# Kernel optimization log

Measured on AMD Instinct MI355X. Metric: run time of the kernel, lower is better.

## Reference

```python
import jax, jax.numpy as jnp
import numpy as np

T = 17            # tensor side -> 289 flat channels
C = T * T
EPS = 1e-5


def tconv(x, W1, W2, b, stride):
    """Tucker-2 tensor conv: per offset (i,j) OUT = W1[i,j] @ X @ W2[i,j].
    x: [B, a*bt, H, W]; W1: [kh,kw,T,a]; W2: [kh,kw,bt,T]; b: [289].
    Equivalent dense kernel K[(p,q),(a,b),i,j] = W1[i,j,p,a]*W2[i,j,b,q]."""
    kh, kw, _, a = W1.shape
    bt = W2.shape[2]
    K = jnp.einsum('ijpa,ijbq->pqabij', W1, W2).reshape(C, a * bt, kh, kw)
    pad = (kh - 1) // 2
    y = jax.lax.conv_general_dilated(
        x, K, (stride, stride), [(pad, pad), (pad, pad)],
        dimension_numbers=('NCHW', 'OIHW', 'NCHW'))
    return y + b.reshape(1, C, 1, 1)


def bn(x, g, bta):
    # training-mode BN over flattened 17x17 tensor channels (biased var)
    m = jnp.mean(x, axis=(0, 2, 3), keepdims=True)
    v = jnp.var(x, axis=(0, 2, 3), keepdims=True)
    return g.reshape(1, -1, 1, 1) * (x - m) * jax.lax.rsqrt(v + EPS) + bta.reshape(1, -1, 1, 1)


def prelu(x, a):
    return jnp.where(x >= 0, x, a * x)


def setup_inputs() -> dict:
    key = jax.random.key(0)
    ks = jax.random.split(key, 8)
    x = jax.random.normal(ks[0], (32, 3, 160, 160), dtype=jnp.float32)
    s = 0.1
    feat_W1 = jax.random.normal(ks[1], (3, 3, T, 3), dtype=jnp.float32) * s
    feat_W2 = jax.random.normal(ks[2], (3, 3, 1, T), dtype=jnp.float32) * s
    feat_b = jnp.zeros((C,), dtype=jnp.float32)
    # 27 1x1 convs: shortcuts 0..8, block k uses 9+2k and 10+2k
    c11_W1 = jax.random.normal(ks[3], (27, 1, 1, T, T), dtype=jnp.float32) * s
    c11_W2 = jax.random.normal(ks[4], (27, 1, 1, T, T), dtype=jnp.float32) * s
    c11_b = jnp.zeros((27, C), dtype=jnp.float32)
    # 9 3x3 convs (one per block)
    c33_W1 = jax.random.normal(ks[5], (9, 3, 3, T, T), dtype=jnp.float32) * s
    c33_W2 = jax.random.normal(ks[6], (9, 3, 3, T, T), dtype=jnp.float32) * s
    c33_b = jnp.zeros((9, C), dtype=jnp.float32)
    # 37 BNs: 0=features, 1+j shortcut j, 10+3k..12+3k block k
    bn_g = jnp.ones((37, C), dtype=jnp.float32)
    bn_bt = jnp.zeros((37, C), dtype=jnp.float32)
    # 19 PReLUs: 0=features, block k uses 1+2k, 2+2k
    prelu_a = jnp.full((19,), 0.25, dtype=jnp.float32)
    return {"x": x, "feat_W1": feat_W1, "feat_W2": feat_W2, "feat_b": feat_b,
            "c11_W1": c11_W1, "c11_W2": c11_W2, "c11_b": c11_b,
            "c33_W1": c33_W1, "c33_W2": c33_W2, "c33_b": c33_b,
            "bn_g": bn_g, "bn_bt": bn_bt, "prelu_a": prelu_a}


def reference(x, feat_W1, feat_W2, feat_b, c11_W1, c11_W2, c11_b,
              c33_W1, c33_W2, c33_b, bn_g, bn_bt, prelu_a):
    # features: 3x3 s2 tensor conv [3,1]->[17,17], BN, PReLU
    h = tconv(x, feat_W1, feat_W2, feat_b, 2)
    h = prelu(bn(h, bn_g[0], bn_bt[0]), prelu_a[0])
    # 9 residual blocks; blocks 0,1 downsample by 2
    for k in range(9):
        s = 2 if k < 2 else 1
        i1, i2 = 9 + 2 * k, 10 + 2 * k
        j = 10 + 3 * k
        idn = bn(tconv(h, c11_W1[k], c11_W2[k], c11_b[k], s), bn_g[1 + k], bn_bt[1 + k])
        y = prelu(bn(tconv(h, c11_W1[i1], c11_W2[i1], c11_b[i1], 1), bn_g[j], bn_bt[j]), prelu_a[1 + 2 * k])
        y = prelu(bn(tconv(y, c33_W1[k], c33_W2[k], c33_b[k], s), bn_g[j + 1], bn_bt[j + 1]), prelu_a[2 + 2 * k])
        y = bn(tconv(y, c11_W1[i2], c11_W2[i2], c11_b[i2], 1), bn_g[j + 2], bn_bt[j + 2])
        h = y + idn
    return h  # [B, 289, 20, 20] == torch [B,1,20,20,17,17] flattened
```

## Files before the change

### kernel.cpp

```cpp
#include <hip/hip_runtime.h>
#include <hip/hip_bf16.h>

#define EPS 1e-5f
#define NB 256
#define CSTR 292
#define PST 580

typedef __hip_bfloat16 bf16;
typedef short s16x8 __attribute__((ext_vector_type(8)));
typedef float f32x4 __attribute__((ext_vector_type(4)));
typedef unsigned short u16x4 __attribute__((ext_vector_type(4)));
typedef unsigned short u16x8 __attribute__((ext_vector_type(8)));

__device__ inline float bf2f(unsigned short u) {
    union { unsigned int i; float f; } z; z.i = ((unsigned int)u) << 16; return z.f;
}
__device__ inline unsigned short f2bf(float f) {
    union { bf16 h; unsigned short u; } z; z.h = __float2bfloat16(f); return z.u;
}
__device__ inline unsigned short f2bf_trunc(float f) {
    union { float f; unsigned int u; } z; z.f = f; return (unsigned short)(z.u >> 16);
}
__device__ inline float ldv(const bf16* p, long i) { return __bfloat162float(p[i]); }
__device__ inline float ldv(const float* p, long i) { return p[i]; }

__device__ __forceinline__ void prep_frag(const float* w1, const float* w2,
                                          bf16* o, int kt, int nt, int l) {
#pragma unroll
    for (int e = 0; e < 8; ++e) {
        int k = kt * 32 + ((l >> 4) << 3) + e;
        int n = nt * 16 + (l & 15);
        float v = 0.f;
        if (k < 289 && n < 289)
            v = w1[(n / 17) * 17 + (k / 17)] * w2[(k % 17) * 17 + (n % 17)];
        o[e] = __float2bfloat16(v);
    }
}

__global__ void prep11_all_k(const float* __restrict__ W1all, const float* __restrict__ W2all,
                             bf16* __restrict__ Bsw) {
    int bi = blockIdx.x;
    int cv = bi / 190, r = bi - cv * 190;
    int kt = r / 19, nt = r - kt * 19;
    prep_frag(W1all + (size_t)cv * 289, W2all + (size_t)cv * 289,
              Bsw + (size_t)bi * 512 + threadIdx.x * 8, kt, nt, threadIdx.x);
}

__global__ void prep33_k(const float* __restrict__ W1, const float* __restrict__ W2,
                         bf16* __restrict__ Bsw) {
    int bi = blockIdx.x;
    int tap = bi / 190; int r = bi - tap * 190;
    int kt = r / 19, nt = r - kt * 19;
    prep_frag(W1 + (size_t)tap * 289, W2 + (size_t)tap * 289,
              Bsw + (size_t)bi * 512 + threadIdx.x * 8, kt, nt, threadIdx.x);
}

__global__ void prep33all_k(const float* __restrict__ W1, const float* __restrict__ W2,
                            bf16* __restrict__ Bsw) {
    int fi = blockIdx.x * 4 + (threadIdx.x >> 6);
    int l = threadIdx.x & 63;
    int kb = fi / 1710, r = fi - kb * 1710;
    int tap = r / 190; int rr = r - tap * 190;
    int kt = rr / 19, nt = rr - kt * 19;
    const float* w1 = W1 + (long)(kb + 1) * 9 * 289 + (long)tap * 289;
    const float* w2 = W2 + (long)(kb + 1) * 9 * 289 + (long)tap * 289;
    prep_frag(w1, w2, Bsw + (size_t)fi * 512 + l * 8, kt, nt, l);
}

__global__ void feat_k(const float* __restrict__ x, bf16* __restrict__ out,
                       const float* __restrict__ W1, const float* __restrict__ W2) {
    __shared__ float W1s[459], W2s[153];
    int tid = threadIdx.x;
    for (int i = tid; i < 459; i += 256) W1s[i] = W1[i];
    for (int i = tid; i < 153; i += 256) W2s[i] = W2[i];
    __syncthreads();
    const long N = 204800L * 17;
    for (long idx = (long)blockIdx.x * 256 + tid; idx < N; idx += 524288L) {
        int pix = (int)(idx / 17), p = (int)(idx - (long)pix * 17);
        int b = pix / 6400; int rr = pix - b * 6400;
        int oh = rr / 80, ow = rr - oh * 80;
        float y[17];
#pragma unroll
        for (int q = 0; q < 17; ++q) y[q] = 0.f;
        for (int di = 0; di < 3; ++di) {
            int ih = oh * 2 + di - 1;
            if (ih < 0 || ih >= 160) continue;
            for (int dj = 0; dj < 3; ++dj) {
                int iw = ow * 2 + dj - 1;
                if (iw < 0 || iw >= 160) continue;
                int k = di * 3 + dj;
                long xb = (long)b * 76800 + ih * 160 + iw;
                float dot = W1s[(k * 17 + p) * 3 + 0] * x[xb]
                          + W1s[(k * 17 + p) * 3 + 1] * x[xb + 25600]
                          + W1s[(k * 17 + p) * 3 + 2] * x[xb + 51200];
#pragma unroll
                for (int q = 0; q < 17; ++q) y[q] += dot * W2s[k * 17 + q];
            }
        }
        long op = (long)pix * CSTR + p * 17;
#pragma unroll
        for (int q = 0; q < 17; ++q) out[op + q] = __float2bfloat16(y[q]);
    }
}

template <typename TI, typename TO, int TAPS, bool DUAL, int MT>
__global__ __launch_bounds__(256, MT == 2 ? 3 : 5) void gemm_k(
    const TI* __restrict__ in1, const TI* __restrict__ in2, TO* __restrict__ out,
    const bf16* __restrict__ Bs, const float* __restrict__ scshAll, int bn1, int bn2,
    const float* __restrict__ alphaPtr, float* __restrict__ partial,
    int Hin, int Win, int Hout, int Wout, int stride) {
    constexpr int MROWS = 16 * MT;
    constexpr int SITS = (37 * MROWS + 255) / 256;
    static_assert(MROWS * 304 * sizeof(TO) <= 2 * MROWS * 640, "epilogue must fit As");
    __shared__ char As[2 * MROWS * 640];
    __shared__ float sc1[296], sh1[296];
    __shared__ float sc2[DUAL ? 296 : 1], sh2[DUAL ? 296 : 1];
    __shared__ long gb00[MROWS];
    __shared__ int ihw0[MROWS];
    int tid = threadIdx.x;
    int HWin = Hin * Win, HWout = Hout * Wout;
    int pix0 = blockIdx.x * MROWS;
    for (int i = tid; i < 296; i += 256) {
        int cc = i < 289 ? i : 0;
        sc1[i] = scshAll[bn1 * 578 + cc]; sh1[i] = scshAll[bn1 * 578 + 289 + cc];
        if constexpr (DUAL) {
            sc2[i] = scshAll[bn2 * 578 + cc]; sh2[i] = scshAll[bn2 * 578 + 289 + cc];
        }
    }
    if (tid < MROWS) {
        int op = pix0 + tid;
        int b = op / HWout; int rr = op - b * HWout;
        int oh = rr / Wout, ow = rr - oh * Wout;
        int ih0 = oh * stride + (TAPS == 9 ? -1 : 0);
        int iw0 = ow * stride + (TAPS == 9 ? -1 : 0);
        gb00[tid] = ((long)b * HWin + (long)ih0 * Win + iw0) * CSTR;
        ihw0[tid] = ((ih0 + 1) << 16) | (iw0 + 1);
    }
    if (tid < 8 * MROWS) {
        int half = tid / (4 * MROWS), r = (tid >> 2) & (MROWS - 1), c = tid & 3;
        int byte = (r * 640 + 576 + c * 16) ^ ((r & 7) << 4);
        *(u16x8*)(As + half * (MROWS * 640) + byte) = (u16x8){0, 0, 0, 0, 0, 0, 0, 0};
    }
    float alpha = DUAL ? 0.f : *alphaPtr;
    int w = tid >> 6, l = tid & 63;
    int nt0 = w * 5;
    int lane_n = l & 15;
    int kbyte = (l >> 4) << 4;
    f32x4 acc[MT][5];
#pragma unroll
    for (int m = 0; m < MT; ++m)
#pragma unroll
        for (int j = 0; j < 5; ++j) acc[m][j] = (f32x4){0.f, 0.f, 0.f, 0.f};
    __syncthreads();

    bool cact[SITS]; int cih[SITS], ciw[SITS], cwb[SITS], ck0[SITS]; long cgb[SITS];
#pragma unroll
    for (int it = 0; it < SITS; ++it) {
        int cid = it * 256 + tid;
        cact[it] = cid < 37 * MROWS;
        int row = cact[it] ? cid / 37 : 0;
        int j = cid - row * 37;
        ck0[it] = j * 8;
        cgb[it] = gb00[row] + j * 8;
        int pk = ihw0[row];
        cih[it] = (pk >> 16) - 1; ciw[it] = (pk & 0xffff) - 1;
        cwb[it] = (row * 640 + j * 16) ^ ((row & 7) << 4);
    }
    bool vld[SITS];
    u16x4 rh1[SITS][2]; f32x4 rf1[SITS][2];
    u16x4 rh2[DUAL ? SITS : 1][2]; f32x4 rf2[DUAL ? SITS : 1][2];

    auto LOAD = [&](int tap) {
        int di = (TAPS == 9) ? tap / 3 : 0;
        int dj = (TAPS == 9) ? tap - di * 3 : 0;
        long toff = (long)(di * Win + dj) * CSTR;
#pragma unroll
        for (int it = 0; it < SITS; ++it) {
            vld[it] = false;
            if (cact[it]) {
                int ih = cih[it] + di, iw = ciw[it] + dj;
                if (ih >= 0 && ih < Hin && iw >= 0 && iw < Win) {
                    vld[it] = true;
                    long gb = cgb[it] + toff;
                    if constexpr (sizeof(TI) == 2) {
                        rh1[it][0] = *(const u16x4*)((const bf16*)in1 + gb);
                        rh1[it][1] = *(const u16x4*)((const bf16*)in1 + gb + 4);
                        if constexpr (DUAL) {
                            rh2[it][0] = *(const u16x4*)((const bf16*)in2 + gb);
                            rh2[it][1] = *(const u16x4*)((const bf16*)in2 + gb + 4);
                        }
                    } else {
                        rf1[it][0] = *(const f32x4*)((const float*)in1 + gb);
                        rf1[it][1] = *(const f32x4*)((const float*)in1 + gb + 4);
                        if constexpr (DUAL) {
                            rf2[it][0] = *(const f32x4*)((const float*)in2 + gb);
                            rf2[it][1] = *(const f32x4*)((const float*)in2 + gb + 4);
                        }
                    }
                }
            }
        }
    };

    auto WRITE = [&]() {
#pragma unroll
        for (int it = 0; it < SITS; ++it) {
            if (!cact[it]) continue;
            float v[8];
            if (vld[it]) {
                int k0 = ck0[it];
                float r[8];
                if constexpr (sizeof(TI) == 2) {
#pragma unroll
                    for (int e = 0; e < 4; ++e) {
                        r[e] = bf2f(rh1[it][0][e]); r[4 + e] = bf2f(rh1[it][1][e]);
                    }
                } else {
#pragma unroll
                    for (int e = 0; e < 4; ++e) {
                        r[e] = rf1[it][0][e]; r[4 + e] = rf1[it][1][e];
                    }
                }
#pragma unroll
                for (int e = 0; e < 8; ++e) v[e] = sc1[k0 + e] * r[e] + sh1[k0 + e];
                if constexpr (DUAL) {
                    float q[8];
                    if constexpr (sizeof(TI) == 2) {
#pragma unroll
                        for (int e = 0; e < 4; ++e) {
                            q[e] = bf2f(rh2[it][0][e]); q[4 + e] = bf2f(rh2[it][1][e]);
                        }
                    } else {
#pragma unroll
                        for (int e = 0; e < 4; ++e) {
                            q[e] = rf2[it][0][e]; q[4 + e] = rf2[it][1][e];
                        }
                    }
#pragma unroll
                    for (int e = 0; e < 8; ++e) v[e] += sc2[k0 + e] * q[e] + sh2[k0 + e];
                } else {
#pragma unroll
                    for (int e = 0; e < 8; ++e) v[e] = v[e] >= 0.f ? v[e] : alpha * v[e];
                }
#pragma unroll
                for (int e = 0; e < 8; ++e) if (ck0[it] + e > 288) v[e] = 0.f;
            } else {
#pragma unroll
                for (int e = 0; e < 8; ++e) v[e] = 0.f;
            }
            u16x4 hi0, hi1, lo0, lo1;
#pragma unroll
            for (int e = 0; e < 4; ++e) {
                unsigned short h = f2bf(v[e]);
                hi0[e] = h; lo0[e] = f2bf_trunc(v[e] - bf2f(h));
                unsigned short h2 = f2bf(v[4 + e]);
                hi1[e] = h2; lo1[e] = f2bf_trunc(v[4 + e] - bf2f(h2));
            }
            int byte = cwb[it];
            *(u16x4*)(As + byte) = hi0;
            *(u16x4*)(As + byte + 8) = hi1;
            *(u16x4*)(As + MROWS * 640 + byte) = lo0;
            *(u16x4*)(As + MROWS * 640 + byte + 8) = lo1;
        }
    };

    LOAD(0);
#pragma unroll 1
    for (int tap = 0; tap < TAPS; ++tap) {
        WRITE();
        if (tap + 1 < TAPS) LOAD(tap + 1);
        __syncthreads();
        const bf16* bp = Bs + (size_t)tap * 97280 + (size_t)l * 8;
        int swz = (lane_n & 7) << 4;
        __builtin_amdgcn_s_setprio(1);
#pragma unroll 2
        for (int kt = 0; kt < 10; ++kt) {
            s16x8 ah[MT], al[MT];
#pragma unroll
            for (int m = 0; m < MT; ++m) {
                int ro = ((m * 16 + lane_n) * 640 + kbyte + kt * 64) ^ swz;
                ah[m] = *(const s16x8*)(As + ro);
                al[m] = *(const s16x8*)(As + MROWS * 640 + ro);
            }
#pragma unroll
            for (int j = 0; j < 5; ++j) {
                if (j < 4 || w < 3) {
                    s16x8 bfr = *(const s16x8*)(bp + (size_t)(kt * 19 + nt0 + j) * 512);
#pragma unroll
                    for (int m = 0; m < MT; ++m) {
                        acc[m][j] = __builtin_amdgcn_mfma_f32_16x16x32_bf16(
                            ah[m], bfr, acc[m][j], 0, 0, 0);
                        acc[m][j] = __builtin_amdgcn_mfma_f32_16x16x32_bf16(
                            al[m], bfr, acc[m][j], 0, 0, 0);
                    }
                }
            }
        }
        __builtin_amdgcn_s_setprio(0);
        __syncthreads();
    }
    {
#pragma unroll
        for (int j = 0; j < 5; ++j) {
            float s = 0.f, ss = 0.f;
            if (j < 4 || w < 3) {
#pragma unroll
                for (int m = 0; m < MT; ++m)
#pragma unroll
                    for (int e = 0; e < 4; ++e) {
                        float v = acc[m][j][e];
                        s += v; ss += v * v;
                    }
            }
            s += __shfl_xor(s, 16); ss += __shfl_xor(ss, 16);
            s += __shfl_xor(s, 32); ss += __shfl_xor(ss, 32);
            int n = (nt0 + j) * 16 + lane_n;
            if (l < 16 && n < 289 && (j < 4 || w < 3)) {
                partial[(long)blockIdx.x * PST + n] = s;
                partial[(long)blockIdx.x * PST + 290 + n] = ss;
            }
        }
    }
    {
        TO* ep = (TO*)As;
        int re = (l >> 4) << 2;
#pragma unroll
        for (int m = 0; m < MT; ++m) {
#pragma unroll
            for (int j = 0; j < 5; ++j) {
                if (j < 4 || w < 3) {
                    int n = (nt0 + j) * 16 + lane_n;
#pragma unroll
                    for (int e = 0; e < 4; ++e) {
                        if constexpr (sizeof(TO) == 2)
                            ep[(m * 16 + re + e) * 304 + n] = __float2bfloat16(acc[m][j][e]);
                        else
                            ((float*)ep)[(m * 16 + re + e) * 304 + n] = acc[m][j][e];
                    }
                }
            }
        }
        __syncthreads();
        for (int cid = tid; cid < MROWS * 73; cid += 256) {
            int row = cid / 73, j = cid - row * 73;
            long g = (long)(pix0 + row) * CSTR + j * 4;
            if constexpr (sizeof(TO) == 2) {
                u16x4 v = *(const u16x4*)((const bf16*)ep + row * 304 + j * 4);
                *(u16x4*)((bf16*)out + g) = v;
            } else {
                f32x4 v = *(const f32x4*)((const float*)ep + row * 304 + j * 4);
                *(f32x4*)((float*)out + g) = v;
            }
        }
    }
}

__global__ __launch_bounds__(256, 3) void gemm2_k(
    const float* __restrict__ in1, const float* __restrict__ in2,
    float* __restrict__ out1, float* __restrict__ out2,
    const bf16* __restrict__ Bs1, const bf16* __restrict__ Bs2,
    const float* __restrict__ scshAll, int bn1, int bn2,
    float* __restrict__ partial1, float* __restrict__ partial2) {
    constexpr int MROWS = 16;
    __shared__ char As[2 * MROWS * 640];
    __shared__ float sc1[296], sh1[296], sc2[296], sh2[296];
    int tid = threadIdx.x;
    for (int i = tid; i < 296; i += 256) {
        int cc = i < 289 ? i : 0;
        sc1[i] = scshAll[bn1 * 578 + cc]; sh1[i] = scshAll[bn1 * 578 + 289 + cc];
        sc2[i] = scshAll[bn2 * 578 + cc]; sh2[i] = scshAll[bn2 * 578 + 289 + cc];
    }
    if (tid < 128) {
        int half = tid >> 6, r = (tid >> 2) & 15, c = tid & 3;
        int byte = (r * 640 + 576 + c * 16) ^ ((r & 7) << 4);
        *(u16x8*)(As + half * (MROWS * 640) + byte) = (u16x8){0, 0, 0, 0, 0, 0, 0, 0};
    }
    int pix0 = blockIdx.x * MROWS;
    int w = tid >> 6, l = tid & 63;
    int nt0 = w * 5, lane_n = l & 15, kbyte = (l >> 4) << 4;
    f32x4 acc1[5], acc2[5];
#pragma unroll
    for (int j = 0; j < 5; ++j) {
        acc1[j] = (f32x4){0.f, 0.f, 0.f, 0.f};
        acc2[j] = (f32x4){0.f, 0.f, 0.f, 0.f};
    }
    __syncthreads();
#pragma unroll
    for (int it = 0; it < 3; ++it) {
        int cid = it * 256 + tid;
        if (cid < 592) {
            int row = cid / 37, j = cid - row * 37, k0 = j * 8;
            long gb = (long)(pix0 + row) * CSTR + k0;
            f32x4 a = *(const f32x4*)(in1 + gb), b = *(const f32x4*)(in1 + gb + 4);
            f32x4 c = *(const f32x4*)(in2 + gb), d = *(const f32x4*)(in2 + gb + 4);
            float v[8];
#pragma unroll
            for (int e = 0; e < 4; ++e) {
                v[e] = sc1[k0 + e] * a[e] + sh1[k0 + e] + sc2[k0 + e] * c[e] + sh2[k0 + e];
                v[4 + e] = sc1[k0 + 4 + e] * b[e] + sh1[k0 + 4 + e]
                         + sc2[k0 + 4 + e] * d[e] + sh2[k0 + 4 + e];
            }
#pragma unroll
            for (int e = 0; e < 8; ++e) if (k0 + e > 288) v[e] = 0.f;
            u16x4 hi0, hi1, lo0, lo1;
#pragma unroll
            for (int e = 0; e < 4; ++e) {
                unsigned short h = f2bf(v[e]);
                hi0[e] = h; lo0[e] = f2bf_trunc(v[e] - bf2f(h));
                unsigned short h2 = f2bf(v[4 + e]);
                hi1[e] = h2; lo1[e] = f2bf_trunc(v[4 + e] - bf2f(h2));
            }
            int byte = (row * 640 + j * 16) ^ ((row & 7) << 4);
            *(u16x4*)(As + byte) = hi0;
            *(u16x4*)(As + byte + 8) = hi1;
            *(u16x4*)(As + MROWS * 640 + byte) = lo0;
            *(u16x4*)(As + MROWS * 640 + byte + 8) = lo1;
        }
    }
    __syncthreads();
    const bf16* bp1 = Bs1 + (size_t)l * 8;
    const bf16* bp2 = Bs2 + (size_t)l * 8;
    int swz = (lane_n & 7) << 4;
    __builtin_amdgcn_s_setprio(1);
#pragma unroll 2
    for (int kt = 0; kt < 10; ++kt) {
        int ro = (lane_n * 640 + kbyte + kt * 64) ^ swz;
        s16x8 ah = *(const s16x8*)(As + ro);
        s16x8 al = *(const s16x8*)(As + MROWS * 640 + ro);
#pragma unroll
        for (int j = 0; j < 5; ++j) {
            if (j < 4 || w < 3) {
                size_t fo = (size_t)(kt * 19 + nt0 + j) * 512;
                s16x8 b1 = *(const s16x8*)(bp1 + fo);
                acc1[j] = __builtin_amdgcn_mfma_f32_16x16x32_bf16(ah, b1, acc1[j], 0, 0, 0);
                acc1[j] = __builtin_amdgcn_mfma_f32_16x16x32_bf16(al, b1, acc1[j], 0, 0, 0);
                s16x8 b2 = *(const s16x8*)(bp2 + fo);
                acc2[j] = __builtin_amdgcn_mfma_f32_16x16x32_bf16(ah, b2, acc2[j], 0, 0, 0);
                acc2[j] = __builtin_amdgcn_mfma_f32_16x16x32_bf16(al, b2, acc2[j], 0, 0, 0);
            }
        }
    }
    __builtin_amdgcn_s_setprio(0);
    __syncthreads();
#pragma unroll
    for (int j = 0; j < 5; ++j) {
        float s1 = 0.f, q1 = 0.f, s2 = 0.f, q2 = 0.f;
        if (j < 4 || w < 3) {
#pragma unroll
            for (int e = 0; e < 4; ++e) {
                float v1 = acc1[j][e]; s1 += v1; q1 += v1 * v1;
                float v2 = acc2[j][e]; s2 += v2; q2 += v2 * v2;
            }
        }
        s1 += __shfl_xor(s1, 16); q1 += __shfl_xor(q1, 16);
        s1 += __shfl_xor(s1, 32); q1 += __shfl_xor(q1, 32);
        s2 += __shfl_xor(s2, 16); q2 += __shfl_xor(q2, 16);
        s2 += __shfl_xor(s2, 32); q2 += __shfl_xor(q2, 32);
        int n = (nt0 + j) * 16 + lane_n;
        if (l < 16 && n < 289 && (j < 4 || w < 3)) {
            partial1[(long)blockIdx.x * PST + n] = s1;
            partial1[(long)blockIdx.x * PST + 290 + n] = q1;
            partial2[(long)blockIdx.x * PST + n] = s2;
            partial2[(long)blockIdx.x * PST + 290 + n] = q2;
        }
    }
    float* ep = (float*)As;
    int re = (l >> 4) << 2;
#pragma unroll
    for (int pass = 0; pass < 2; ++pass) {
        const f32x4* ac = pass ? acc2 : acc1;
        float* op = pass ? out2 : out1;
#pragma unroll
        for (int j = 0; j < 5; ++j) {
            if (j < 4 || w < 3) {
                int n = (nt0 + j) * 16 + lane_n;
#pragma unroll
                for (int e = 0; e < 4; ++e) ep[(re + e) * 304 + n] = ac[j][e];
            }
        }
        __syncthreads();
        for (int cid = tid; cid < MROWS * 73; cid += 256) {
            int row = cid / 73, j = cid - row * 73;
            long g = (long)(pix0 + row) * CSTR + j * 4;
            f32x4 v = *(const f32x4*)(ep + row * 304 + j * 4);
            *(f32x4*)(op + g) = v;
        }
        __syncthreads();
    }
}

__global__ void stats_k(const bf16* __restrict__ t, float* __restrict__ partial, int npix) {
    int c = threadIdx.x;
    if (c >= 289) return;
    float s = 0.f, ss = 0.f;
    for (int pix = blockIdx.x; pix < npix; pix += NB) {
        float v = ldv(t, (long)pix * CSTR + c);
        s += v; ss += v * v;
    }
    partial[(long)blockIdx.x * PST + c] = s;
    partial[(long)blockIdx.x * PST + 290 + c] = ss;
}

__device__ __forceinline__ void fin_one(const float* partial, const float* g,
                                        const float* bt, float* scshAll,
                                        int bnid, float invN, int GN, int c) {
    float s = 0.f, ss = 0.f;
    for (int k = threadIdx.x; k < GN; k += 256) {
        s += partial[(long)k * PST + c];
        ss += partial[(long)k * PST + 290 + c];
    }
    for (int o = 32; o; o >>= 1) { s += __shfl_down(s, o); ss += __shfl_down(ss, o); }
    __shared__ float ls[4], lss[4];
    int w = threadIdx.x >> 6;
    if ((threadIdx.x & 63) == 0) { ls[w] = s; lss[w] = ss; }
    __syncthreads();
    if (threadIdx.x == 0) {
        s = ls[0] + ls[1] + ls[2] + ls[3];
        ss = lss[0] + lss[1] + lss[2] + lss[3];
        float m = s * invN;
        float v = ss * invN - m * m;
        float sc = g[c] * rsqrtf(v + EPS);
        scshAll[bnid * 578 + c] = sc;
        scshAll[bnid * 578 + 289 + c] = bt[c] - m * sc;
    }
}

__global__ void finalize_k(const float* __restrict__ partial, const float* __restrict__ g,
                           const float* __restrict__ bt, float* __restrict__ scshAll,
                           int bnid, float invN, int GN) {
    fin_one(partial, g, bt, scshAll, bnid, invN, GN, blockIdx.x);
}

__global__ void finalize2v_k(const float* __restrict__ pA, const float* __restrict__ pB,
                             const float* __restrict__ gAll, const float* __restrict__ btAll,
                             float* __restrict__ scshAll, int bnA, int bnB,
                             float invA, int GNa, float invB, int GNb) {
    int q = blockIdx.x / 289, c = blockIdx.x - q * 289;
    const float* p = q ? pB : pA;
    int bnid = q ? bnB : bnA;
    fin_one(p, gAll + bnid * 289, btAll + bnid * 289, scshAll, bnid,
            q ? invB : invA, q ? GNb : GNa, c);
}

__global__ void final_k(const float* __restrict__ y3, const float* __restrict__ idn,
                        float* __restrict__ out, const float* __restrict__ scshAll,
                        int bnY, int bnI) {
    __shared__ float T[32][305];
    int bi = blockIdx.x;
    int b = bi / 13, t0 = (bi - (bi / 13) * 13) * 32;
    int tid = threadIdx.x;
    int nhw = 400 - t0; if (nhw > 32) nhw = 32;
    for (int idx = tid; idx < 32 * 304; idx += 256) {
        int hwl = idx / 304, c = idx - hwl * 304;
        float v = 0.f;
        if (hwl < nhw && c < 289) {
            long pix = (long)b * 400 + t0 + hwl;
            v = scshAll[bnY * 578 + c] * y3[pix * CSTR + c] + scshAll[bnY * 578 + 289 + c]
              + scshAll[bnI * 578 + c] * idn[pix * CSTR + c] + scshAll[bnI * 578 + 289 + c];
        }
        T[hwl][c] = v;
    }
    __syncthreads();
    for (int idx = tid; idx < 289 * 32; idx += 256) {
        int c = idx >> 5, hwl = idx & 31;
        if (hwl < nhw)
            out[((long)b * 289 + c) * 400 + t0 + hwl] = T[hwl][c];
    }
}

extern "C" void kernel_launch(void* const* d_in, const int* in_sizes, int n_in,
                              void* d_out, int out_size, void* d_ws, size_t ws_size,
                              hipStream_t stream) {
    const float* x     = (const float*)d_in[0];
    const float* fW1   = (const float*)d_in[1];
    const float* fW2   = (const float*)d_in[2];
    const float* c11W1 = (const float*)d_in[4];
    const float* c11W2 = (const float*)d_in[5];
    const float* c33W1 = (const float*)d_in[7];
    const float* c33W2 = (const float*)d_in[8];
    const float* bng   = (const float*)d_in[10];
    const float* bnbt  = (const float*)d_in[11];
    const float* pa    = (const float*)d_in[12];
    float* outp = (float*)d_out;

    char* base = (char*)d_ws;
    bf16*  A    = (bf16*)base;
    bf16*  Bb   = (bf16*)(base + 119603200L);
    bf16*  Cb   = (bf16*)(base + 149504000L);
    float* scsh = (float*)(base + 179404800L);
    bf16*  B33s = (bf16*)(base + 179490368L);
    size_t need = 181241408L;
    if (ws_size < need) return;
    float* D = (float*)base;
    float* E = (float*)(base + 14950400L);
    float* F = (float*)(base + 29900800L);
    float* partialA = (float*)(base + 50000000L);
    bf16*  B33all   = (bf16*)(base + 100000000L);

    float* partial = (float*)d_out;
    bf16*  B11all  = (bf16*)((char*)d_out + 7424000L);
    float* partial2 = partial + 800L * PST;
    float* partialBig = (float*)Cb;

    const float inv80 = 1.f / 204800.f, inv40 = 1.f / 51200.f, inv20 = 1.f / 12800.f;

#define B11(cv) (B11all + (size_t)(cv) * 97280)
#define B33A(cv) (B33all + (size_t)((cv) - 1) * 875520)
#define FIN(P, bnid, invN, GN) finalize_k<<<dim3(289), dim3(256), 0, stream>>>( \
        (P), bng + (bnid) * 289, bnbt + (bnid) * 289, scsh, (bnid), (invN), (GN))

    prep11_all_k<<<dim3(27 * 190), dim3(64), 0, stream>>>(c11W1, c11W2, B11all);

    feat_k<<<dim3(2048), dim3(256), 0, stream>>>(x, A, fW1, fW2);
    stats_k<<<dim3(NB), dim3(320), 0, stream>>>(A, partial, 204800);
    FIN(partial, 0, inv80, NB);

    gemm_k<bf16, bf16, 1, false, 2><<<dim3(1600), dim3(256), 0, stream>>>(
        A, nullptr, Bb, B11(0), scsh, 0, 0, pa + 0, partial, 80, 80, 40, 40, 2);
    gemm_k<bf16, bf16, 1, false, 2><<<dim3(6400), dim3(256), 0, stream>>>(
        A, nullptr, A, B11(9), scsh, 0, 0, pa + 0, partialBig, 80, 80, 80, 80, 1);
    finalize2v_k<<<dim3(578), dim3(256), 0, stream>>>(
        partial, partialBig, bng, bnbt, scsh, 1, 10, inv40, 1600, inv80, 6400);
    prep33_k<<<dim3(1710), dim3(64), 0, stream>>>(c33W1, c33W2, B33s);
    gemm_k<bf16, bf16, 9, false, 2><<<dim3(1600), dim3(256), 0, stream>>>(
        A, nullptr, Cb, B33s, scsh, 10, 0, pa + 1, partial, 80, 80, 40, 40, 2);
    prep33all_k<<<dim3(3420), dim3(256), 0, stream>>>(c33W1, c33W2, B33all);
    FIN(partial, 11, inv40, 1600);
    gemm_k<bf16, bf16, 1, false, 2><<<dim3(1600), dim3(256), 0, stream>>>(
        Cb, nullptr, Cb, B11(10), scsh, 11, 0, pa + 2, partial, 40, 40, 40, 40, 1);
    FIN(partial, 12, inv40, 1600);

    gemm_k<bf16, float, 1, true, 1><<<dim3(800), dim3(256), 0, stream>>>(
        Cb, Bb, D, B11(1), scsh, 12, 1, nullptr, partialA, 40, 40, 20, 20, 2);
    gemm_k<bf16, bf16, 1, true, 2><<<dim3(1600), dim3(256), 0, stream>>>(
        Cb, Bb, Cb, B11(11), scsh, 12, 1, nullptr, partial, 40, 40, 40, 40, 1);
    finalize2v_k<<<dim3(578), dim3(256), 0, stream>>>(
        partialA, partial, bng, bnbt, scsh, 2, 13, inv20, 800, inv40, 1600);
    gemm_k<bf16, float, 9, false, 2><<<dim3(400), dim3(256), 0, stream>>>(
        Cb, nullptr, E, B33A(1), scsh, 13, 0, pa + 3, partial, 40, 40, 20, 20, 2);
    FIN(partial, 14, inv20, 400);
    gemm_k<float, float, 1, false, 1><<<dim3(800), dim3(256), 0, stream>>>(
        E, nullptr, E, B11(12), scsh, 14, 0, pa + 4, partial, 20, 20, 20, 20, 1);
    FIN(partial, 15, inv20, 800);

    float *X = E, *Y = D, *Z = F;
    for (int k = 2; k < 9; ++k) {
        gemm2_k<<<dim3(800), dim3(256), 0, stream>>>(
            X, Y, Z, X, B11(k), B11(9 + 2 * k), scsh, 9 + 3 * k, k, partial, partial2);
        finalize2v_k<<<dim3(578), dim3(256), 0, stream>>>(
            partial, partial2, bng, bnbt, scsh, 1 + k, 10 + 3 * k,
            inv20, 800, inv20, 800);
        gemm_k<float, float, 9, false, 2><<<dim3(400), dim3(256), 0, stream>>>(
            X, nullptr, Y, B33A(k), scsh, 10 + 3 * k, 0, pa + 1 + 2 * k, partial,
            20, 20, 20, 20, 1);
        FIN(partial, 11 + 3 * k, inv20, 400);
        gemm_k<float, float, 1, false, 1><<<dim3(800), dim3(256), 0, stream>>>(
            Y, nullptr, Y, B11(10 + 2 * k), scsh, 11 + 3 * k, 0, pa + 2 + 2 * k, partial,
            20, 20, 20, 20, 1);
        FIN(partial, 12 + 3 * k, inv20, 800);
        float* t = X; X = Y; Y = Z; Z = t;
    }
    final_k<<<dim3(416), dim3(256), 0, stream>>>(X, Y, outp, scsh, 36, 9);
}
```

Measured before the change: 2.214 ms.

## Fuse first BN statistics into feature conv and stage output through LDS

The feature tensor conv now accumulates per-channel sum and sum-of-squares in registers while it computes, reduces them through shared-memory atomics, and writes per-block partials. The separate stats kernel, which re-read the whole 204800x292 bf16 activation, is removed. Outputs are staged in a shared tile of 15 pixels and written with coalesced 8-byte stores instead of scattered 2-byte stores. The trade-off is more partials (2048 instead of 256) for finalize to reduce, extra barriers per tile, and one of 256 threads left idle.

```diff
diff --git a/kernel.cpp b/kernel.cpp
--- a/kernel.cpp
+++ b/kernel.cpp
@@ -2,9 +2,9 @@
 #include <hip/hip_bf16.h>
 
 #define EPS 1e-5f
-#define NB 256
 #define CSTR 292
 #define PST 580
+#define FPIX 15
 
 typedef __hip_bfloat16 bf16;
 typedef short s16x8 __attribute__((ext_vector_type(8)));
@@ -21,8 +21,6 @@
 __device__ inline unsigned short f2bf_trunc(float f) {
     union { float f; unsigned int u; } z; z.f = f; return (unsigned short)(z.u >> 16);
 }
-__device__ inline float ldv(const bf16* p, long i) { return __bfloat162float(p[i]); }
-__device__ inline float ldv(const float* p, long i) { return p[i]; }
 
 __device__ __forceinline__ void prep_frag(const float* w1, const float* w2,
                                           bf16* o, int kt, int nt, int l) {
@@ -67,39 +65,77 @@
     prep_frag(w1, w2, Bsw + (size_t)fi * 512 + l * 8, kt, nt, l);
 }
 
-__global__ void feat_k(const float* __restrict__ x, bf16* __restrict__ out,
-                       const float* __restrict__ W1, const float* __restrict__ W2) {
+__global__ __launch_bounds__(256) void feat_k(
+    const float* __restrict__ x, bf16* __restrict__ out,
+    const float* __restrict__ W1, const float* __restrict__ W2,
+    float* __restrict__ partial) {
     __shared__ float W1s[459], W2s[153];
+    __shared__ float S[289], SS[289];
+    __shared__ bf16 T[FPIX][292];
     int tid = threadIdx.x;
     for (int i = tid; i < 459; i += 256) W1s[i] = W1[i];
     for (int i = tid; i < 153; i += 256) W2s[i] = W2[i];
-    __syncthreads();
-    const long N = 204800L * 17;
-    for (long idx = (long)blockIdx.x * 256 + tid; idx < N; idx += 524288L) {
-        int pix = (int)(idx / 17), p = (int)(idx - (long)pix * 17);
-        int b = pix / 6400; int rr = pix - b * 6400;
-        int oh = rr / 80, ow = rr - oh * 80;
-        float y[17];
-#pragma unroll
-        for (int q = 0; q < 17; ++q) y[q] = 0.f;
-        for (int di = 0; di < 3; ++di) {
-            int ih = oh * 2 + di - 1;
-            if (ih < 0 || ih >= 160) continue;
-            for (int dj = 0; dj < 3; ++dj) {
-                int iw = ow * 2 + dj - 1;
-                if (iw < 0 || iw >= 160) continue;
-                int k = di * 3 + dj;
-                long xb = (long)b * 76800 + ih * 160 + iw;
-                float dot = W1s[(k * 17 + p) * 3 + 0] * x[xb]
-                          + W1s[(k * 17 + p) * 3 + 1] * x[xb + 25600]
-                          + W1s[(k * 17 + p) * 3 + 2] * x[xb + 51200];
-#pragma unroll
-                for (int q = 0; q < 17; ++q) y[q] += dot * W2s[k * 17 + q];
-            }
-        }
-        long op = (long)pix * CSTR + p * 17;
-#pragma unroll
-        for (int q = 0; q < 17; ++q) out[op + q] = __float2bfloat16(y[q]);
+    for (int i = tid; i < 289; i += 256) { S[i] = 0.f; SS[i] = 0.f; }
+    if (tid < FPIX * 3) T[tid / 3][289 + tid % 3] = __float2bfloat16(0.f);
+    int lp = tid / 17, p = tid - lp * 17;
+    bool act = tid < 255;
+    float sacc[17], qacc[17];
+#pragma unroll
+    for (int q = 0; q < 17; ++q) { sacc[q] = 0.f; qacc[q] = 0.f; }
+    const int NT = (204800 + FPIX - 1) / FPIX;
+    __syncthreads();
+    for (int t = blockIdx.x; t < NT; t += gridDim.x) {
+        int pix0 = t * FPIX;
+        int pix = pix0 + lp;
+        if (act && pix < 204800) {
+            int b = pix / 6400; int rr = pix - b * 6400;
+            int oh = rr / 80, ow = rr - oh * 80;
+            float y[17];
+#pragma unroll
+            for (int q = 0; q < 17; ++q) y[q] = 0.f;
+            for (int di = 0; di < 3; ++di) {
+                int ih = oh * 2 + di - 1;
+                if (ih < 0 || ih >= 160) continue;
+                for (int dj = 0; dj < 3; ++dj) {
+                    int iw = ow * 2 + dj - 1;
+                    if (iw < 0 || iw >= 160) continue;
+                    int k = di * 3 + dj;
+                    long xb = (long)b * 76800 + ih * 160 + iw;
+                    float dot = W1s[(k * 17 + p) * 3 + 0] * x[xb]
+                              + W1s[(k * 17 + p) * 3 + 1] * x[xb + 25600]
+                              + W1s[(k * 17 + p) * 3 + 2] * x[xb + 51200];
+#pragma unroll
+                    for (int q = 0; q < 17; ++q) y[q] += dot * W2s[k * 17 + q];
+                }
+            }
+#pragma unroll
+            for (int q = 0; q < 17; ++q) {
+                bf16 h = __float2bfloat16(y[q]);
+                T[lp][p * 17 + q] = h;
+                float vv = __bfloat162float(h);
+                sacc[q] += vv; qacc[q] += vv * vv;
+            }
+        }
+        __syncthreads();
+        int nv = 204800 - pix0; if (nv > FPIX) nv = FPIX;
+        for (int idx = tid; idx < nv * 73; idx += 256) {
+            int row = idx / 73, j = idx - row * 73;
+            *(u16x4*)(out + (long)(pix0 + row) * CSTR + j * 4) =
+                *(const u16x4*)(&T[row][j * 4]);
+        }
+        __syncthreads();
+    }
+    if (act) {
+#pragma unroll
+        for (int q = 0; q < 17; ++q) {
+            atomicAdd(&S[p * 17 + q], sacc[q]);
+            atomicAdd(&SS[p * 17 + q], qacc[q]);
+        }
+    }
+    __syncthreads();
+    for (int i = tid; i < 289; i += 256) {
+        partial[(long)blockIdx.x * PST + i] = S[i];
+        partial[(long)blockIdx.x * PST + 290 + i] = SS[i];
     }
 }
 
@@ -489,18 +525,6 @@
     }
 }
 
-__global__ void stats_k(const bf16* __restrict__ t, float* __restrict__ partial, int npix) {
-    int c = threadIdx.x;
-    if (c >= 289) return;
-    float s = 0.f, ss = 0.f;
-    for (int pix = blockIdx.x; pix < npix; pix += NB) {
-        float v = ldv(t, (long)pix * CSTR + c);
-        s += v; ss += v * v;
-    }
-    partial[(long)blockIdx.x * PST + c] = s;
-    partial[(long)blockIdx.x * PST + 290 + c] = ss;
-}
-
 __device__ __forceinline__ void fin_one(const float* partial, const float* g,
                                         const float* bt, float* scshAll,
                                         int bnid, float invN, int GN, int c) {
@@ -611,9 +635,8 @@
 
     prep11_all_k<<<dim3(27 * 190), dim3(64), 0, stream>>>(c11W1, c11W2, B11all);
 
-    feat_k<<<dim3(2048), dim3(256), 0, stream>>>(x, A, fW1, fW2);
-    stats_k<<<dim3(NB), dim3(320), 0, stream>>>(A, partial, 204800);
-    FIN(partial, 0, inv80, NB);
+    feat_k<<<dim3(2048), dim3(256), 0, stream>>>(x, A, fW1, fW2, partial);
+    FIN(partial, 0, inv80, 2048);
 
     gemm_k<bf16, bf16, 1, false, 2><<<dim3(1600), dim3(256), 0, stream>>>(
         A, nullptr, Bb, B11(0), scsh, 0, 0, pa + 0, partial, 80, 80, 40, 40, 2);
```

New measurement: 1.891 ms. 1.17x faster.
